# Kernel optimization log

Hardware: AMD Instinct MI355X
Metric: run time of the kernel (lower is better)

The kernel has to match this reference:

```python
import jax, jax.numpy as jnp
import numpy as np
import math

B, C, N, T = 16, 32, 500, 10
NH, DK = 8, 8
D = NH * DK  # 64
TT = 6       # tem_size after conv_temp1 (10->6)
EPS = 1e-5


def setup_inputs() -> dict:
    key = jax.random.key(0)
    ks = jax.random.split(key, 32)
    s = 0.05
    rn = lambda k, shp: jax.random.normal(k, shp, dtype=jnp.float32) * s
    return {
        "x": jax.random.normal(ks[0], (B, C, N, T), dtype=jnp.float32),
        "A": jax.random.uniform(ks[1], (N, N), dtype=jnp.float32) / N,
        "conv1_W": rn(ks[2], (32, 32)), "conv1_b": jnp.zeros((32,), jnp.float32),
        "te1_W": rn(ks[3], (64, 32)), "te1_b": jnp.zeros((64,), jnp.float32),
        "convq_W": rn(ks[4], (64, 64, 1, 3)), "convq_b": jnp.zeros((64,), jnp.float32),
        "convk_W": rn(ks[5], (64, 64, 1, 3)), "convk_b": jnp.zeros((64,), jnp.float32),
        "linv_W": rn(ks[6], (64, 64)), "linv_b": jnp.zeros((64,), jnp.float32),
        "lino_W": rn(ks[7], (64, 64)), "lino_b": jnp.zeros((64,), jnp.float32),
        "te2_W": rn(ks[8], (32, 64)), "te2_b": jnp.zeros((32,), jnp.float32),
        "mlp_W": rn(ks[9], (64, 160)), "mlp_b": jnp.zeros((64,), jnp.float32),
        "ct1_W": rn(ks[10], (6, 10)), "ct1_b": jnp.zeros((6,), jnp.float32),
        "tat_c1_W": rn(ks[11], (32,)), "tat_c2_W": rn(ks[12], (500,)),
        "tat_w": rn(ks[13], (500, 32)), "tat_b": jnp.zeros((6, 6), jnp.float32),
        "tat_v": rn(ks[14], (6, 6)),
        "bn1_g": jnp.ones((6,), jnp.float32), "bn1_b": jnp.zeros((6,), jnp.float32),
        "bn2_g": jnp.ones((32,), jnp.float32), "bn2_b": jnp.zeros((32,), jnp.float32),
    }


def _forward(x, A, conv1_W, conv1_b, te1_W, te1_b, convq_W, convq_b, convk_W, convk_b,
             linv_W, linv_b, lino_W, lino_b, te2_W, te2_b, mlp_W, mlp_b, ct1_W, ct1_b,
             tat_c1_W, tat_c2_W, tat_w, tat_b, tat_v, bn1_g, bn1_b, bn2_g, bn2_b):
    b, c, n, t = x.shape
    c1x1 = lambda z, W, bb: jnp.einsum('bchw,oc->bohw', z, W) + bb[None, :, None, None]
    residual = c1x1(x, conv1_W, conv1_b)                      # (B,32,N,T)
    h = c1x1(x, te1_W, te1_b)                                 # (B,64,N,T)
    # --- temporal-context multi-head self-attention (att bias is 0 in source due to bug) ---
    dn = ('NCHW', 'OIHW', 'NCHW')
    q = jax.lax.conv_general_dilated(h, convq_W, (1, 1), ((0, 0), (1, 1)), dimension_numbers=dn) + convq_b[None, :, None, None]
    k = jax.lax.conv_general_dilated(h, convk_W, (1, 1), ((0, 0), (1, 1)), dimension_numbers=dn) + convk_b[None, :, None, None]
    sh = lambda z: z.reshape(b, NH, DK, n, t).transpose(0, 3, 1, 4, 2)  # (B,N,h,T,dk)
    q, k = sh(q), sh(k)
    hp = h.transpose(0, 2, 3, 1)                              # (B,N,T,64)
    v = (hp @ linv_W.T + linv_b).reshape(b, n, t, NH, DK).transpose(0, 1, 3, 2, 4)
    p = jax.nn.softmax(jnp.einsum('bnhtd,bnhsd->bnhts', q, k) / math.sqrt(DK), axis=-1)
    o = jnp.einsum('bnhts,bnhsd->bnhtd', p, v).transpose(0, 1, 3, 2, 4).reshape(b, n, t, D)
    h = (o @ lino_W.T + lino_b).transpose(0, 3, 1, 2)         # (B,64,N,T)
    h = c1x1(h, te2_W, te2_b)                                 # (B,32,N,T)
    # --- multi_gcn_d: static adjacency diffusion + per-timestep attention adjacency ---
    co = h.shape[1]
    xt = h.transpose(0, 3, 2, 1)                              # (B,T,N,C)
    att = jax.nn.softmax(jnp.einsum('btnc,btmc->btnm', xt, xt) / math.sqrt(co), axis=-1)
    outs = [h]
    z = jnp.einsum('btvc,wv->btwc', xt, A); outs.append(z.transpose(0, 3, 2, 1))
    z = jnp.einsum('btvc,wv->btwc', z, A);  outs.append(z.transpose(0, 3, 2, 1))
    z = jnp.einsum('btvc,btwv->btwc', xt, att); outs.append(z.transpose(0, 3, 2, 1))
    z = jnp.einsum('btvc,btwv->btwc', z, att);  outs.append(z.transpose(0, 3, 2, 1))
    hc = c1x1(jnp.concatenate(outs, axis=1), mlp_W, mlp_b)    # (B,64,N,T)
    g = jnp.tanh(hc[:, :co]) * jax.nn.sigmoid(hc[:, co:])     # (B,32,N,10)
    # --- conv_temp1: 1x1 conv over the time axis, 10 -> 6 ---
    g = jnp.einsum('bcnt,st->bcns', g, ct1_W) + ct1_b[None, None, None, :]  # (B,32,N,6)
    # --- TATT_1 temporal attention coefficients ---
    f1 = jnp.einsum('bcnt,c->btn', g, tat_c1_W)               # (B,6,N)
    f2 = jnp.einsum('bcnt,n->bct', g, tat_c2_W)               # (B,32,6)
    logits = jax.nn.sigmoid(jnp.einsum('btn,nc,bcs->bts', f1, tat_w, f2) + tat_b)
    logits = jnp.einsum('pt,bts->bps', tat_v, logits)         # (B,6,6)
    lp = logits.transpose(0, 2, 1)
    mu = lp.mean((0, 2), keepdims=True); var = lp.var((0, 2), keepdims=True)
    lp = (lp - mu) / jnp.sqrt(var + EPS) * bn1_g[None, :, None] + bn1_b[None, :, None]
    coefs = jax.nn.softmax(lp.transpose(0, 2, 1), axis=-1)    # (B,6,6)
    Tc = coefs.transpose(0, 2, 1)
    xo = jnp.einsum('bcnl,blq->bcnq', g, Tc)                  # (B,32,N,6)
    xo = jnp.where(xo > 0, xo, 0.01 * xo) + residual[..., -xo.shape[-1]:]
    mu = xo.mean((0, 2, 3), keepdims=True); var = xo.var((0, 2, 3), keepdims=True)
    return (xo - mu) / jnp.sqrt(var + EPS) * bn2_g[None, :, None, None] + bn2_b[None, :, None, None]


def reference(x, A, conv1_W, conv1_b, te1_W, te1_b, convq_W, convq_b, convk_W, convk_b,
              linv_W, linv_b, lino_W, lino_b, te2_W, te2_b, mlp_W, mlp_b, ct1_W, ct1_b,
              tat_c1_W, tat_c2_W, tat_w, tat_b, tat_v, bn1_g, bn1_b, bn2_g, bn2_b):
    return _forward(x, A, conv1_W, conv1_b, te1_W, te1_b, convq_W, convq_b, convk_W, convk_b,
                    linv_W, linv_b, lino_W, lino_b, te2_W, te2_b, mlp_W, mlp_b, ct1_W, ct1_b,
                    tat_c1_W, tat_c2_W, tat_w, tat_b, tat_v, bn1_g, bn1_b, bn2_g, bn2_b)
```

## Files before the change

### kernel.cpp

```cpp
#include <hip/hip_runtime.h>

typedef unsigned short u16;
typedef unsigned int u32;

__device__ __forceinline__ float b2f(u16 v) { return __uint_as_float((u32)v << 16); }
__device__ __forceinline__ float lopart(u32 u) { return __uint_as_float(u << 16); }
__device__ __forceinline__ float hipart(u32 u) { return __uint_as_float(u & 0xffff0000u); }
__device__ __forceinline__ u16 f2b(float f) {
  u32 u = __float_as_uint(f);
  u32 r = u + 0x7fffu + ((u >> 16) & 1u);
  return (u16)(r >> 16);
}
__device__ __forceinline__ u32 pk2(float a, float b) {
  return (u32)f2b(a) | ((u32)f2b(b) << 16);
}
__device__ __forceinline__ u32 cvtpk(float lo, float hi) {
  u32 r;
  asm("v_cvt_pk_bf16_f32 %0, %1, %2" : "=v"(r) : "v"(lo), "v"(hi));
  return r;
}
__device__ __forceinline__ float rd(const void* p, int i, bool BF) {
  return BF ? b2f(((const u16*)p)[i]) : ((const float*)p)[i];
}

struct Ptrs { const void* p[29]; };

typedef __attribute__((ext_vector_type(8))) short short8;
typedef __attribute__((ext_vector_type(4))) float floatx4;

__global__ __launch_bounds__(256) void k_prep(Ptrs ps, float* __restrict__ Wf,
                                              u16* __restrict__ Abf, float* __restrict__ WT,
                                              u16* __restrict__ WBu, float* __restrict__ stats) {
  bool BF = ((*(const u32*)ps.p[25]) & 0xffffu) != 0;
  int blk = blockIdx.x, tid = threadIdx.x;
  if (blk < 256) {
    int j = blk * 256 + tid;
    if (j >= 65322) return;
    const int SZ[27] = {1024,32,2048,64,12288,64,12288,64,4096,64,4096,64,2048,32,
                        10240,64,60,6,32,500,16000,36,36,6,6,32,32};
    int t = 0, off = 0;
#pragma unroll
    for (int k = 0; k < 27; ++k) {
      if (t == k && j >= off + SZ[k]) { off += SZ[k]; t = k + 1; }
    }
    Wf[j] = rd(ps.p[2 + t], j - off, BF);
  } else if (blk < 1280) {
    int i = (blk - 256) * 256 + tid;
    int r = i >> 9, v = i & 511;
    bool in = (r < 500) && (v < 500);
    u16 o = 0;
    if (in) o = BF ? ((const u16*)ps.p[1])[r * 500 + v] : f2b(((const float*)ps.p[1])[r * 500 + v]);
    Abf[i] = o;
  } else if (blk < 1366) {
    int i = (blk - 1280) * 256 + tid;
    const void* p2  = ps.p[2];
    const void* p4  = ps.p[4];
    const void* p5  = ps.p[5];
    const void* p6  = ps.p[6];
    const void* p7  = ps.p[7];
    const void* p8  = ps.p[8];
    const void* p9  = ps.p[9];
    const void* p10 = ps.p[10];
    const void* p11 = ps.p[11];
    const void* p12 = ps.p[12];
    const void* p13 = ps.p[13];
    const void* p14 = ps.p[14];
    const void* p15 = ps.p[15];
    const void* p16 = ps.p[16];
    if (i < 1024) {
      WT[i] = rd(p2, (i & 31) * 32 + (i >> 5), BF);
    } else if (i < 7168) {
      int j2 = i - 1024;
      int o = j2 & 63, ct = j2 >> 6;
      int c = ct / 3, tap = ct - c * 3;
      float sq = 0.f, sk = 0.f;
      for (int i2 = 0; i2 < 64; ++i2) {
        float te = rd(p4, i2 * 32 + c, BF);
        sq += rd(p6, o * 192 + i2 * 3 + tap, BF) * te;
        sk += rd(p8, o * 192 + i2 * 3 + tap, BF) * te;
      }
      ((u32*)WT)[i] = pk2(sq, sk);
    } else if (i < 7552) {
      int j2 = i - 7168;
      int f = j2 >> 6, o = j2 & 63;
      const void* pw = (f & 1) ? p8 : p6;
      float S0 = 0.f, S1 = 0.f, S2 = 0.f;
      for (int i2 = 0; i2 < 64; ++i2) {
        float tb = rd(p5, i2, BF);
        S0 += rd(pw, o * 192 + i2 * 3 + 0, BF) * tb;
        S1 += rd(pw, o * 192 + i2 * 3 + 1, BF) * tb;
        S2 += rd(pw, o * 192 + i2 * 3 + 2, BF) * tb;
      }
      float r;
      if (f == 0)      r = rd(p7, o, BF) + S0 + S1 + S2;
      else if (f == 1) r = rd(p9, o, BF) + S0 + S1 + S2;
      else if (f < 4)  r = S0;
      else             r = S2;
      WT[i] = r;
    } else if (i < 9600) {
      int j2 = i - 7552;
      int c = j2 >> 6, o = j2 & 63;
      float s = 0.f;
      for (int i2 = 0; i2 < 64; ++i2)
        s += rd(p10, o * 64 + i2, BF) * rd(p4, i2 * 32 + c, BF);
      WT[i] = s;
    } else if (i < 9664) {
      int o = i - 9600;
      float s = rd(p11, o, BF);
      for (int i2 = 0; i2 < 64; ++i2)
        s += rd(p10, o * 64 + i2, BF) * rd(p5, i2, BF);
      WT[i] = s;
    } else if (i < 11712) {
      int j2 = i - 9664;
      int jj = j2 >> 5, c = j2 & 31;
      float s = 0.f;
      for (int o2 = 0; o2 < 64; ++o2)
        s += rd(p14, c * 64 + o2, BF) * rd(p12, o2 * 64 + jj, BF);
      WT[i] = s;
    } else if (i < 11744) {
      int c = i - 11712;
      float s = rd(p15, c, BF);
      for (int o2 = 0; o2 < 64; ++o2)
        s += rd(p14, c * 64 + o2, BF) * rd(p13, o2, BF);
      WT[i] = s;
    } else if (i < 21984) {
      int j2 = i - 11744;
      int j = j2 & 7, lanev = (j2 >> 3) & 63, ct = (j2 >> 9) & 3, kt = j2 >> 11;
      int qv = lanev >> 4, lnv = lanev & 15;
      int o = ct * 16 + lnv, k = kt * 32 + qv * 8 + j;
      WBu[j2] = f2b(rd(p16, o * 160 + k, BF));
    }
  } else {
    if (tid < 64) stats[tid] = 0.f;
  }
}

__global__ __launch_bounds__(256, 4) void k_a2m(const u16* __restrict__ Abf,
                                                u16* __restrict__ A2bf) {
  __shared__ u32 blsT[8192];
  int tid = threadIdx.x;
  int c0 = blockIdx.x * 32;
  for (int i = tid; i < 8192; i += 256) {
    int c = i & 31, h = i >> 5;
    int r0 = 2 * h;
    u32 lo = Abf[r0 * 512 + c0 + c];
    u32 hi = Abf[(r0 + 1) * 512 + c0 + c];
    blsT[c * 256 + (((h & 0xFC) ^ ((c & 15) << 2)) | (h & 3))] = lo | (hi << 16);
  }
  __syncthreads();
  int lane = tid & 63, wave = tid >> 6;
  int q = lane >> 4, ln = lane & 15;
  int rbase = blockIdx.y * 64 + wave * 16;
  const u32* Au = (const u32*)Abf;
  int arow = (rbase + ln) * 256;
  union F8 { u32 u[4]; short8 s; };
  floatx4 acc[2] = {{0.f,0.f,0.f,0.f},{0.f,0.f,0.f,0.f}};
  for (int c2 = 0; c2 < 16; ++c2) {
    int hb = c2 * 16 + q * 4;
    F8 af;
#pragma unroll
    for (int i2 = 0; i2 < 4; ++i2) af.u[i2] = Au[arow + hb + i2];
#pragma unroll
    for (int t2 = 0; t2 < 2; ++t2) {
      int c = t2 * 16 + ln;
      int baseT = c * 256 + (hb ^ ((c & 15) << 2));
      F8 bf;
#pragma unroll
      for (int i2 = 0; i2 < 4; ++i2) bf.u[i2] = blsT[baseT + i2];
      acc[t2] = __builtin_amdgcn_mfma_f32_16x16x32_bf16(af.s, bf.s, acc[t2], 0, 0, 0);
    }
  }
#pragma unroll
  for (int t2 = 0; t2 < 2; ++t2) {
#pragma unroll
    for (int i2 = 0; i2 < 4; ++i2) {
      int r = rbase + q * 4 + i2;
      A2bf[r * 512 + c0 + t2 * 16 + ln] = f2b(acc[t2][i2]);
    }
  }
}

__global__ __launch_bounds__(256, 7) void k_front3(
    const void* __restrict__ xraw, const void* __restrict__ g1, const float* __restrict__ WT,
    const float* __restrict__ c1B,
    float* __restrict__ h3x, float* __restrict__ res6)
{
  __shared__ __align__(16) float arena[4][1440];
  int tid = threadIdx.x;
  int wave = tid >> 6, lane = tid & 63;
  float* Aw = arena[wave];
  int pair = blockIdx.x * 4 + wave;
  int b = pair / 500, n = pair - b * 500;

  const float* c1T  = WT;
  const u32*   qkF  = (const u32*)(WT + 1024);
  const float* bCq  = WT + 7168;
  const float* bCk  = WT + 7232;
  const float* bE0q = WT + 7296;
  const float* bE0k = WT + 7360;
  const float* bE2q = WT + 7424;
  const float* bE2k = WT + 7488;
  const float* vT   = WT + 7552;
  const float* bvp  = WT + 9600;
  const float* otT  = WT + 9664;
  const float* botp = WT + 11712;

  {
    bool BF = ((*(const u32*)g1) & 0xffffu) != 0;
    int c0 = lane >> 1, hf = (lane & 1) * 5;
    int base = ((b * 32 + c0) * 500 + n) * 10 + hf;
    float* dst = Aw + c0 * 12 + hf;
    if (BF) {
      const u16* xp = (const u16*)xraw + base;
#pragma unroll
      for (int k2 = 0; k2 < 5; ++k2) dst[k2] = b2f(xp[k2]);
    } else {
      const float* xp = (const float*)xraw + base;
#pragma unroll
      for (int k2 = 0; k2 < 5; ++k2) dst[k2] = xp[k2];
    }
  }
  __builtin_amdgcn_wave_barrier();

  int cl = lane & 31, th = lane >> 5;

  {
    float r0 = c1B[cl], r1 = r0, r2 = r0;
#pragma unroll 4
    for (int i = 0; i < 32; ++i) {
      float w = c1T[i * 32 + cl];
      const float* xr = Aw + i * 12 + 4 + th * 3;
      r0 += w * xr[0]; r1 += w * xr[1]; r2 += w * xr[2];
    }
    float* rp = res6 + ((b * 32 + cl) * 500 + n) * 6 + th * 3;
    rp[0] = r0; rp[1] = r1; rp[2] = r2;
  }

  float qr[10], kr[10], vr[10];
  {
    float cq = bCq[lane], ck = bCk[lane], bv = bvp[lane];
#pragma unroll
    for (int t = 0; t < 10; ++t) { qr[t] = cq; kr[t] = ck; vr[t] = bv; }
    qr[0] -= bE0q[lane]; kr[0] -= bE0k[lane];
    qr[9] -= bE2q[lane]; kr[9] -= bE2k[lane];
    const u32* qp0 = qkF + lane;
    const float* vp0 = vT + lane;
#pragma unroll 2
    for (int c = 0; c < 32; ++c) {
      const float* xr = Aw + c * 12;
      float4 ha = *(const float4*)xr;
      float4 hb = *(const float4*)(xr + 4);
      float2 hc = *(const float2*)(xr + 8);
      u32 u0 = qp0[c * 192];
      u32 u1 = qp0[c * 192 + 64];
      u32 u2 = qp0[c * 192 + 128];
      float wv = vp0[c * 64];
      float q0 = lopart(u0), q1 = lopart(u1), q2 = lopart(u2);
      float k0 = hipart(u0), k1 = hipart(u1), k2v = hipart(u2);
      float hh[10] = {ha.x, ha.y, ha.z, ha.w, hb.x, hb.y, hb.z, hb.w, hc.x, hc.y};
#pragma unroll
      for (int t = 0; t < 10; ++t) { float c_ = hh[t]; qr[t] += q1 * c_; kr[t] += k1 * c_; vr[t] += wv * c_; }
#pragma unroll
      for (int t = 1; t < 10; ++t) { float c_ = hh[t - 1]; qr[t] += q0 * c_; kr[t] += k0 * c_; }
#pragma unroll
      for (int t = 0; t < 9; ++t) { float c_ = hh[t + 1]; qr[t] += q2 * c_; kr[t] += k2v * c_; }
    }
  }
  __builtin_amdgcn_wave_barrier();
  {
    u32* qu = (u32*)Aw + lane * 5;
    u32* ku = (u32*)Aw + 320 + lane * 5;
#pragma unroll
    for (int m = 0; m < 5; ++m) {
      qu[m] = cvtpk(qr[2 * m], qr[2 * m + 1]);
      ku[m] = cvtpk(kr[2 * m], kr[2 * m + 1]);
    }
  }
  __builtin_amdgcn_wave_barrier();

  {
    const u32* qb = (const u32*)Aw;
    const u32* kb = (const u32*)Aw + 320;
#pragma unroll
    for (int pass = 0; pass < 2; ++pass) {
      int row = pass * 64 + lane;
      if (row < 80) {
        int h8 = (row / 10) * 8, r = row - (row / 10) * 10;
        int rm = r >> 1, rs = r & 1;
        float sv[10];
#pragma unroll
        for (int s = 0; s < 10; ++s) sv[s] = 0.f;
#pragma unroll 2
        for (int d = 0; d < 8; ++d) {
          int jj = h8 + d;
          u32 qu = qb[jj * 5 + rm];
          float qv = rs ? hipart(qu) : lopart(qu);
          const u32* kp2 = kb + jj * 5;
          u32 ka0 = kp2[0], ka1 = kp2[1], ka2 = kp2[2], ka3 = kp2[3], ka4 = kp2[4];
          sv[0] += qv * lopart(ka0); sv[1] += qv * hipart(ka0);
          sv[2] += qv * lopart(ka1); sv[3] += qv * hipart(ka1);
          sv[4] += qv * lopart(ka2); sv[5] += qv * hipart(ka2);
          sv[6] += qv * lopart(ka3); sv[7] += qv * hipart(ka3);
          sv[8] += qv * lopart(ka4); sv[9] += qv * hipart(ka4);
        }
        const float sc_ = 0.35355339059327373f;
        float mx = sv[0];
#pragma unroll
        for (int s = 1; s < 10; ++s) mx = fmaxf(mx, sv[s]);
        float tot = 0.f, ev[10];
#pragma unroll
        for (int s = 0; s < 10; ++s) { ev[s] = __expf((sv[s] - mx) * sc_); tot += ev[s]; }
        float inv = 1.f / tot;
        float* pp = Aw + 640 + row * 10;
#pragma unroll
        for (int s = 0; s < 10; ++s) pp[s] = ev[s] * inv;
      }
    }
  }
  __builtin_amdgcn_wave_barrier();

  {
    const float* pb = Aw + 640 + (lane >> 3) * 100;
    float orr[10];
#pragma unroll
    for (int t = 0; t < 10; ++t) {
      const float* pr = pb + t * 10;
      float a = 0.f;
#pragma unroll
      for (int s = 0; s < 10; ++s) a += pr[s] * vr[s];
      orr[t] = a;
    }
    float* op = Aw + lane * 12;
    *(float4*)op       = make_float4(orr[0], orr[1], orr[2], orr[3]);
    *(float4*)(op + 4) = make_float4(orr[4], orr[5], orr[6], orr[7]);
    *(float2*)(op + 8) = make_float2(orr[8], orr[9]);
  }
  __builtin_amdgcn_wave_barrier();

  {
    float bt2 = botp[cl];
    float a5[5];
#pragma unroll
    for (int k2 = 0; k2 < 5; ++k2) a5[k2] = bt2;
    const float* tp0 = otT + cl;
    const float* base = Aw + th * 5;
#pragma unroll 2
    for (int j = 0; j < 64; ++j) {
      float w = tp0[j * 32];
      const float* lp = base + j * 12;
#pragma unroll
      for (int k2 = 0; k2 < 5; ++k2) a5[k2] += w * lp[k2];
    }
    int t0 = th * 5;
#pragma unroll
    for (int k2 = 0; k2 < 5; ++k2)
      h3x[((b * 10 + t0 + k2) * 500 + n) * 32 + cl] = a5[k2];
  }
}

__global__ __launch_bounds__(256, 4) void k_z12m(const float* __restrict__ h3x,
    const u16* __restrict__ Abf, const u16* __restrict__ A2bf,
    float* __restrict__ z1x, float* __restrict__ z2x) {
  __shared__ u32 xlsT[8192];
  int tid = threadIdx.x, bt = blockIdx.x;
  const float* src = h3x + bt * 16000;
  for (int i = tid; i < 8192; i += 256) {
    int n = i & 31, h = i >> 5;
    int r0 = 2 * h;
    float v0 = (r0 < 500) ? src[r0 * 32 + n] : 0.f;
    float v1 = (r0 + 1 < 500) ? src[(r0 + 1) * 32 + n] : 0.f;
    xlsT[n * 256 + (((h & 0xFC) ^ ((n & 15) << 2)) | (h & 3))] = cvtpk(v0, v1);
  }
  __syncthreads();
  int lane = tid & 63, wave = tid >> 6;
  int q = lane >> 4, ln = lane & 15;
  int rbase = blockIdx.y * 64 + wave * 16;
  const u32* Au = (const u32*)Abf;
  const u32* A2u = (const u32*)A2bf;
  int arow = (rbase + ln) * 256;
  union F8 { u32 u[4]; short8 s; };
  floatx4 acc1[2] = {{0.f,0.f,0.f,0.f},{0.f,0.f,0.f,0.f}};
  floatx4 acc2[2] = {{0.f,0.f,0.f,0.f},{0.f,0.f,0.f,0.f}};
  for (int c2 = 0; c2 < 16; ++c2) {
    int hb = c2 * 16 + q * 4;
    F8 a1f, a2f;
#pragma unroll
    for (int i2 = 0; i2 < 4; ++i2) {
      a1f.u[i2] = Au[arow + hb + i2];
      a2f.u[i2] = A2u[arow + hb + i2];
    }
#pragma unroll
    for (int t2 = 0; t2 < 2; ++t2) {
      int n = t2 * 16 + ln;
      int baseT = n * 256 + (hb ^ ((n & 15) << 2));
      F8 bf;
#pragma unroll
      for (int i2 = 0; i2 < 4; ++i2) bf.u[i2] = xlsT[baseT + i2];
      acc1[t2] = __builtin_amdgcn_mfma_f32_16x16x32_bf16(a1f.s, bf.s, acc1[t2], 0, 0, 0);
      acc2[t2] = __builtin_amdgcn_mfma_f32_16x16x32_bf16(a2f.s, bf.s, acc2[t2], 0, 0, 0);
    }
  }
  int outb = bt * 16000;
#pragma unroll
  for (int t2 = 0; t2 < 2; ++t2) {
#pragma unroll
    for (int i2 = 0; i2 < 4; ++i2) {
      int r = rbase + q * 4 + i2;
      if (r < 500) {
        z1x[outb + r * 32 + t2 * 16 + ln] = acc1[t2][i2];
        z2x[outb + r * 32 + t2 * 16 + ln] = acc2[t2][i2];
      }
    }
  }
}

__global__ __launch_bounds__(256, 2) void k_attn2(const float* __restrict__ keys,
                                                  const float* __restrict__ vals,
                                                  float* __restrict__ outp) {
  __shared__ u32 kls[10240];
  __shared__ u32 vls[8192];
  __shared__ u32 aux[1216];
  int tid = threadIdx.x, bt = blockIdx.x, yh = blockIdx.y;
  const float* kb = keys + bt * 16000;
  const float* vb = vals + bt * 16000;
  for (int i = tid; i < 8192; i += 256) {
    int r = i >> 4, cu = i & 15;
    float2 g = make_float2(0.f, 0.f);
    if (r < 500) g = *(const float2*)(kb + r * 32 + cu * 2);
    kls[r * 20 + cu] = cvtpk(g.x, g.y);
    int n = i & 31, h = i >> 5;
    int r0 = 2 * h;
    float v0 = (r0 < 500) ? vb[r0 * 32 + n] : 0.f;
    float v1 = (r0 + 1 < 500) ? vb[(r0 + 1) * 32 + n] : 0.f;
    vls[n * 256 + (((h & 0xFC) ^ ((n & 15) << 2)) | (h & 3))] = cvtpk(v0, v1);
  }
  __syncthreads();
  int lane = tid & 63, wave = tid >> 6;
  int q = lane >> 4, ln = lane & 15;
  int wrow = wave >> 1, ch = wave & 1;
  float* smx = (float*)(aux + 1088);
  float* sms = (float*)(aux + 1152);
  u32* myp = aux + wave * 272;
  float* zex = (float*)aux;
  u16* pw = (u16*)myp;
  union F8 { u32 u[4]; short8 s; };
  const float sc = 0.17677669529663687f;
  int outb = bt * 16000;
  for (int chunk = 0; chunk < 8; ++chunk) {
    int rbase = yh * 256 + chunk * 32 + wrow * 16;
    F8 af;
    {
      int r = rbase + ln;
      int wbase = r * 20 + q * 4;
#pragma unroll
      for (int i2 = 0; i2 < 4; ++i2)
        af.u[i2] = kls[wbase + i2];
    }
    floatx4 acc[16];
#pragma unroll
    for (int ctl = 0; ctl < 16; ++ctl) {
      int r2 = (ch * 16 + ctl) * 16 + ln;
      int wb2 = r2 * 20 + q * 4;
      F8 bf;
#pragma unroll
      for (int i2 = 0; i2 < 4; ++i2)
        bf.u[i2] = kls[wb2 + i2];
      acc[ctl] = __builtin_amdgcn_mfma_f32_16x16x32_bf16(af.s, bf.s,
                (floatx4){0.f, 0.f, 0.f, 0.f}, 0, 0, 0);
    }
    if (ch == 1 && ln >= 4) {
#pragma unroll
      for (int i2 = 0; i2 < 4; ++i2) acc[15][i2] = -1e30f;
    }
    float m[4];
#pragma unroll
    for (int i2 = 0; i2 < 4; ++i2) {
      float mm = -1e30f;
#pragma unroll
      for (int ctl = 0; ctl < 16; ++ctl) mm = fmaxf(mm, acc[ctl][i2]);
#pragma unroll
      for (int d = 1; d < 16; d <<= 1) mm = fmaxf(mm, __shfl_xor(mm, d));
      m[i2] = mm;
    }
    if (ln == 0) {
#pragma unroll
      for (int i2 = 0; i2 < 4; ++i2) smx[wave * 16 + q * 4 + i2] = m[i2];
    }
    __syncthreads();
    float sp[4];
#pragma unroll
    for (int i2 = 0; i2 < 4; ++i2) {
      float mm = fmaxf(m[i2], smx[(wave ^ 1) * 16 + q * 4 + i2]);
      float s = 0.f;
#pragma unroll
      for (int ctl = 0; ctl < 16; ++ctl) {
        float e = __expf((acc[ctl][i2] - mm) * sc);
        acc[ctl][i2] = e; s += e;
      }
#pragma unroll
      for (int d = 1; d < 16; d <<= 1) s += __shfl_xor(s, d);
      sp[i2] = s;
    }
    if (ln == 0) {
#pragma unroll
      for (int i2 = 0; i2 < 4; ++i2) sms[wave * 16 + q * 4 + i2] = sp[i2];
    }
    __syncthreads();
    float inv[4];
#pragma unroll
    for (int i2 = 0; i2 < 4; ++i2)
      inv[i2] = 1.f / (sp[i2] + sms[(wave ^ 1) * 16 + q * 4 + i2]);
    floatx4 zacc[2] = {{0.f,0.f,0.f,0.f},{0.f,0.f,0.f,0.f}};
    for (int c2l = 0; c2l < 8; ++c2l) {
#pragma unroll
      for (int t2 = 0; t2 < 2; ++t2) {
        int ctl = c2l * 2 + t2;
#pragma unroll
        for (int i2 = 0; i2 < 4; ++i2)
          pw[(q * 4 + i2) * 34 + t2 * 16 + ln] = f2b(acc[ctl][i2]);
      }
      __builtin_amdgcn_wave_barrier();
      F8 pa;
#pragma unroll
      for (int i2 = 0; i2 < 4; ++i2) pa.u[i2] = myp[ln * 17 + q * 4 + i2];
      int hb = (ch * 8 + c2l) * 16 + q * 4;
#pragma unroll
      for (int t2 = 0; t2 < 2; ++t2) {
        int n = t2 * 16 + ln;
        int baseT = n * 256 + (hb ^ ((n & 15) << 2));
        F8 bf;
#pragma unroll
        for (int i2 = 0; i2 < 4; ++i2) bf.u[i2] = vls[baseT + i2];
        zacc[t2] = __builtin_amdgcn_mfma_f32_16x16x32_bf16(pa.s, bf.s, zacc[t2], 0, 0, 0);
      }
      __builtin_amdgcn_wave_barrier();
    }
    __syncthreads();
    if (ch) {
#pragma unroll
      for (int t2 = 0; t2 < 2; ++t2)
#pragma unroll
        for (int i2 = 0; i2 < 4; ++i2)
          zex[wrow * 544 + (q * 4 + i2) * 34 + t2 * 16 + ln] = zacc[t2][i2];
    }
    __syncthreads();
    if (!ch) {
#pragma unroll
      for (int t2 = 0; t2 < 2; ++t2) {
#pragma unroll
        for (int i2 = 0; i2 < 4; ++i2) {
          int r = rbase + q * 4 + i2;
          if (r < 500) {
            float vsum = zacc[t2][i2] + zex[wrow * 544 + (q * 4 + i2) * 34 + t2 * 16 + ln];
            outp[outb + r * 32 + t2 * 16 + ln] = vsum * inv[i2];
          }
        }
      }
    }
  }
}

__global__ __launch_bounds__(256, 2) void k_gate(
    const float* __restrict__ h3x, const float* __restrict__ z1x, const float* __restrict__ z2x,
    const float* __restrict__ z3x, const float* __restrict__ z4x,
    const u32* __restrict__ WBq, const float* __restrict__ mlpB,
    const float* __restrict__ ct1W, const float* __restrict__ ct1B,
    float* __restrict__ g2w)
{
  __shared__ u32 wlds[5120];
  int tid = threadIdx.x;
  for (int i = tid; i < 5120; i += 256) wlds[i] = WBq[i];
  __syncthreads();
  int lane = tid & 63, wave = tid >> 6;
  int q = lane >> 4, ln = lane & 15;
  int b = blockIdx.y;
  int n0 = blockIdx.x * 32 + wave * 8;
  int nA = n0 + (ln & 7);
  int tAb = ln >> 3;
  int nD = n0 + (q & 1) * 4;
  int tDb = q >> 1;
  float g2a[4][2][6];
#pragma unroll
  for (int i = 0; i < 4; ++i)
#pragma unroll
    for (int ch = 0; ch < 2; ++ch)
#pragma unroll
      for (int s = 0; s < 6; ++s) g2a[i][ch][s] = 0.f;
  float bias[4];
#pragma unroll
  for (int ct = 0; ct < 4; ++ct) bias[ct] = mlpB[ct * 16 + ln];
  union F8 { u32 u[4]; short8 s; };
  for (int tile = 0; tile < 5; ++tile) {
    int tA = tile * 2 + tAb;
    int offA = (((b * 10 + tA) * 500) + nA) * 32 + q * 8;
    floatx4 acc[4];
#pragma unroll
    for (int ct = 0; ct < 4; ++ct) acc[ct] = (floatx4){bias[ct], bias[ct], bias[ct], bias[ct]};
#pragma unroll
    for (int kt = 0; kt < 5; ++kt) {
      const float* sp = kt == 0 ? h3x : kt == 1 ? z1x : kt == 2 ? z2x : kt == 3 ? z3x : z4x;
      float4 a0 = *(const float4*)(sp + offA);
      float4 a1 = *(const float4*)(sp + offA + 4);
      F8 af;
      af.u[0] = cvtpk(a0.x, a0.y);
      af.u[1] = cvtpk(a0.z, a0.w);
      af.u[2] = cvtpk(a1.x, a1.y);
      af.u[3] = cvtpk(a1.z, a1.w);
#pragma unroll
      for (int ct = 0; ct < 4; ++ct) {
        F8 bfr;
        const u32* wp = wlds + (((kt * 4 + ct) << 6) + lane) * 4;
#pragma unroll
        for (int i2 = 0; i2 < 4; ++i2) bfr.u[i2] = wp[i2];
        acc[ct] = __builtin_amdgcn_mfma_f32_16x16x32_bf16(af.s, bfr.s, acc[ct], 0, 0, 0);
      }
    }
    int tD = tile * 2 + tDb;
    float c6[6];
#pragma unroll
    for (int s = 0; s < 6; ++s) c6[s] = ct1W[s * 10 + tD];
#pragma unroll
    for (int i = 0; i < 4; ++i) {
      float e0 = __expf(2.f * acc[0][i]);
      float g0 = ((e0 - 1.f) / (e0 + 1.f)) * (1.f / (1.f + __expf(-acc[2][i])));
      float e1 = __expf(2.f * acc[1][i]);
      float g1 = ((e1 - 1.f) / (e1 + 1.f)) * (1.f / (1.f + __expf(-acc[3][i])));
#pragma unroll
      for (int s = 0; s < 6; ++s) {
        g2a[i][0][s] += g0 * c6[s];
        g2a[i][1][s] += g1 * c6[s];
      }
    }
  }
#pragma unroll
  for (int i = 0; i < 4; ++i)
#pragma unroll
    for (int ch = 0; ch < 2; ++ch)
#pragma unroll
      for (int s = 0; s < 6; ++s)
        g2a[i][ch][s] += __shfl_xor(g2a[i][ch][s], 32);
  if (q < 2) {
#pragma unroll
    for (int i = 0; i < 4; ++i) {
      int n = nD + i;
      if (n < 500) {
#pragma unroll
        for (int ch = 0; ch < 2; ++ch) {
          int c = ln + ch * 16;
          float* gp = g2w + ((b * 32 + c) * 500 + n) * 6;
#pragma unroll
          for (int s = 0; s < 6; ++s) gp[s] = g2a[i][ch][s] + ct1B[s];
        }
      }
    }
  }
}

__global__ __launch_bounds__(256) void k_f12(const float* __restrict__ g2w,
                                             const float* __restrict__ tc1W,
                                             const float* __restrict__ c2W,
                                             float* __restrict__ f1w, float* __restrict__ f2w) {
  int blk = blockIdx.x, tid = threadIdx.x;
  if (blk < 188) {
    int i = blk * 256 + tid;
    if (i >= 48000) return;
    int b = i / 3000, rem = i - b * 3000, s = rem / 500, n = rem - s * 500;
    float a = 0.f;
    for (int c = 0; c < 32; ++c) a += g2w[((b * 32 + c) * 500 + n) * 6 + s] * tc1W[c];
    f1w[(b * 6 + s) * 500 + n] = a;
  } else {
    int pb = (blk - 188) * 4 + (tid >> 6);
    int b = pb >> 5, c = pb & 31, lane = tid & 63;
    float acc[6];
#pragma unroll
    for (int t = 0; t < 6; ++t) acc[t] = 0.f;
    for (int n = lane; n < 500; n += 64) {
      float w = c2W[n];
      const float* gp = g2w + ((b * 32 + c) * 500 + n) * 6;
#pragma unroll
      for (int t = 0; t < 6; ++t) acc[t] += w * gp[t];
    }
#pragma unroll
    for (int t = 0; t < 6; ++t)
      for (int off = 32; off; off >>= 1) acc[t] += __shfl_xor(acc[t], off);
    if (lane == 0) {
#pragma unroll
      for (int t = 0; t < 6; ++t) f2w[(b * 32 + c) * 6 + t] = acc[t];
    }
  }
}

__global__ __launch_bounds__(256) void k_tatt(
    const float* __restrict__ f1w, const float* __restrict__ tatw,
    const float* __restrict__ f2w, const float* __restrict__ tatb, const float* __restrict__ tatv,
    float* __restrict__ lg2w)
{
  __shared__ float mid[192];
  __shared__ float lgt[36];
  int b = blockIdx.x, tid = threadIdx.x;
  if (tid < 192) {
    int t = tid >> 5, c = tid & 31;
    float a = 0.f;
    const float* f1p = f1w + (b * 6 + t) * 500;
    for (int n = 0; n < 500; ++n) a += f1p[n] * tatw[n * 32 + c];
    mid[t * 32 + c] = a;
  }
  __syncthreads();
  if (tid < 36) {
    int t = tid / 6, s = tid - t * 6;
    float a = tatb[t * 6 + s];
    for (int c = 0; c < 32; ++c) a += mid[t * 32 + c] * f2w[(b * 32 + c) * 6 + s];
    lgt[t * 6 + s] = 1.f / (1.f + expf(-a));
  }
  __syncthreads();
  if (tid < 36) {
    int p = tid / 6, s = tid - p * 6;
    float a = 0.f;
#pragma unroll
    for (int t2 = 0; t2 < 6; ++t2) a += tatv[p * 6 + t2] * lgt[t2 * 6 + s];
    lg2w[(b * 6 + p) * 6 + s] = a;
  }
}

__global__ __launch_bounds__(128) void k_coefs(const float* __restrict__ lg2w,
    const float* __restrict__ bn1g, const float* __restrict__ bn1b, float* __restrict__ tcw) {
  __shared__ float mu[6], iv[6], gg[6], bb[6];
  int tid = threadIdx.x;
  if (tid < 6) {
    float s = 0.f, sq = 0.f;
    for (int b = 0; b < 16; ++b)
      for (int q = 0; q < 6; ++q) {
        float v = lg2w[(b * 6 + q) * 6 + tid];
        s += v; sq += v * v;
      }
    float m = s / 96.f;
    mu[tid] = m;
    iv[tid] = rsqrtf(sq / 96.f - m * m + 1e-5f);
    gg[tid] = bn1g[tid]; bb[tid] = bn1b[tid];
  }
  __syncthreads();
  for (int idx = tid; idx < 96; idx += 128) {
    int b = idx / 6, q = idx - b * 6;
    float v[6], mx = -1e30f;
#pragma unroll
    for (int l = 0; l < 6; ++l) {
      v[l] = (lg2w[(b * 6 + q) * 6 + l] - mu[l]) * iv[l] * gg[l] + bb[l];
      mx = fmaxf(mx, v[l]);
    }
    float tot = 0.f;
#pragma unroll
    for (int l = 0; l < 6; ++l) { v[l] = expf(v[l] - mx); tot += v[l]; }
    float inv = 1.f / tot;
#pragma unroll
    for (int l = 0; l < 6; ++l) tcw[(b * 6 + l) * 6 + q] = v[l] * inv;
  }
}

__global__ __launch_bounds__(256) void k_xo(const float* __restrict__ g2w,
    const float* __restrict__ res6, const float* __restrict__ tcw,
    float* __restrict__ xow, float* __restrict__ stats) {
  __shared__ float Tcl[36];
  __shared__ float redS[32][8], redQ[32][8];
  int b = blockIdx.x, chunk = blockIdx.y, tid = threadIdx.x;
  if (tid < 36) Tcl[tid] = tcw[b * 36 + tid];
  __syncthreads();
  int c = tid & 31, sub = tid >> 5;
  int n0 = chunk * 50;
  float s = 0.f, sq = 0.f;
  for (int idx = sub; idx < 300; idx += 8) {
    int nl = idx / 6, q = idx - nl * 6;
    int n = n0 + nl;
    int base = ((b * 32 + c) * 500 + n) * 6;
    const float* gp = g2w + base;
    float xv = 0.f;
#pragma unroll
    for (int l = 0; l < 6; ++l) xv += gp[l] * Tcl[l * 6 + q];
    xv = xv > 0.f ? xv : 0.01f * xv;
    xv += res6[base + q];
    xow[base + q] = xv;
    s += xv; sq += xv * xv;
  }
  redS[c][sub] = s; redQ[c][sub] = sq;
  __syncthreads();
  if (sub == 0) {
    float ts = 0.f, tq = 0.f;
#pragma unroll
    for (int k = 0; k < 8; ++k) { ts += redS[c][k]; tq += redQ[c][k]; }
    atomicAdd(&stats[c], ts);
    atomicAdd(&stats[32 + c], tq);
  }
}

__global__ __launch_bounds__(256) void k_out(const float* __restrict__ xow,
    const float* __restrict__ stats, const float* __restrict__ g2c, const float* __restrict__ b2c,
    float* __restrict__ out) {
  int base = (blockIdx.x * 256 + threadIdx.x) * 4;
#pragma unroll
  for (int k = 0; k < 4; ++k) {
    int i = base + k;
    int c = (i / 3000) & 31;
    float m = stats[c] * (1.f / 48000.f);
    float var = stats[32 + c] * (1.f / 48000.f) - m * m;
    out[i] = (xow[i] - m) * rsqrtf(var + 1e-5f) * g2c[c] + b2c[c];
  }
}

extern "C" void kernel_launch(void* const* d_in, const int* in_sizes, int n_in,
                              void* d_out, int out_size, void* d_ws, size_t ws_size,
                              hipStream_t stream)
{
  (void)in_sizes; (void)out_size;

  float* ws = (float*)d_ws;
  float* Af   = ws;
  float* Wf   = Af + 250000;
  float* A2   = Wf + 65536;
  float* h3x  = A2 + 250000;
  float* z1x  = h3x + 2560000;
  float* z2x  = z1x + 2560000;
  float* z3x  = z2x + 2560000;
  float* z4x  = z3x + 2560000;
  float* res6 = z4x + 2560000;
  float* g2w  = res6 + 1536000;
  float* f1w  = g2w + 1536000;
  float* f2w  = f1w + 48000;
  float* lg2w = f2w + 3072;
  float* tcw  = lg2w + 576;
  float* stats= tcw + 576;
  float* xow  = z1x;
  u16*   Abf  = (u16*)g2w;
  u16*   A2bf = (u16*)(g2w + 131072);
  float* WTp  = g2w + 262144;
  u16*   WBu  = (u16*)f1w;
  if (ws_size < (size_t)16489952 * sizeof(float)) return;

  const float* c1B  = Wf + 1024;
  const float* mlpB = Wf + 48512;
  const float* ct1W = Wf + 48576;
  const float* ct1B = Wf + 48636;
  const float* tc1W = Wf + 48642;
  const float* tc2W = Wf + 48674;
  const float* tatw = Wf + 49174;
  const float* tatb = Wf + 65174;
  const float* tatv = Wf + 65210;
  const float* bn1g = Wf + 65246;
  const float* bn1b = Wf + 65252;
  const float* bn2g = Wf + 65258;
  const float* bn2b = Wf + 65290;

  Ptrs ps;
  for (int i = 0; i < 29; ++i) ps.p[i] = (i < n_in) ? d_in[i] : d_in[0];

  k_prep <<<dim3(1367),    256, 0, stream>>>(ps, Wf, Abf, WTp, WBu, stats);
  k_a2m  <<<dim3(16, 8),   256, 0, stream>>>(Abf, A2bf);
  k_front3<<<dim3(2000),   256, 0, stream>>>(ps.p[0], ps.p[25], WTp, c1B, h3x, res6);
  k_z12m <<<dim3(160, 8),  256, 0, stream>>>(h3x, Abf, A2bf, z1x, z2x);
  k_attn2<<<dim3(160, 2),  256, 0, stream>>>(h3x, h3x, z3x);
  k_attn2<<<dim3(160, 2),  256, 0, stream>>>(h3x, z3x, z4x);
  k_gate <<<dim3(16, 16),  256, 0, stream>>>(h3x, z1x, z2x, z3x, z4x,
                                             (const u32*)WBu, mlpB, ct1W, ct1B, g2w);
  k_f12  <<<dim3(316),     256, 0, stream>>>(g2w, tc1W, tc2W, f1w, f2w);
  k_tatt <<<dim3(16),      256, 0, stream>>>(f1w, tatw, f2w, tatb, tatv, lg2w);
  k_coefs<<<dim3(1),       128, 0, stream>>>(lg2w, bn1g, bn1b, tcw);
  k_xo   <<<dim3(16, 10),  256, 0, stream>>>(g2w, res6, tcw, xow, stats);
  k_out  <<<dim3(1500),    256, 0, stream>>>(xow, stats, bn2g, bn2b, (float*)d_out);
}
```

Measured before the change: 401.1 us.

## Compute front Q/K/V projections with bf16 MFMA instead of scalar FMA loops

Replaces the per-lane scalar FMA accumulation of the fused te1+conv_q/conv_k/linear_v projections in k_front3 with 16x16x32 bf16 MFMA tiles. It does this by building a time-shifted im2col of x in LDS, while k_prep emits the projection weights pre-swizzled into MFMA fragment layout along with per-boundary bias classes. Attention probabilities and V are now stored as bf16 in LDS. Shared memory grows and the occupancy hint drops from 7 to 5 blocks. The change adds bf16 rounding of Q/K/V inputs and probabilities.

```diff
diff --git a/kernel.cpp b/kernel.cpp
--- a/kernel.cpp
+++ b/kernel.cpp
@@ -33,6 +33,20 @@
                                               u16* __restrict__ WBu, float* __restrict__ stats) {
   bool BF = ((*(const u32*)ps.p[25]) & 0xffffu) != 0;
   int blk = blockIdx.x, tid = threadIdx.x;
+  const void* p2  = ps.p[2];
+  const void* p4  = ps.p[4];
+  const void* p5  = ps.p[5];
+  const void* p6  = ps.p[6];
+  const void* p7  = ps.p[7];
+  const void* p8  = ps.p[8];
+  const void* p9  = ps.p[9];
+  const void* p10 = ps.p[10];
+  const void* p11 = ps.p[11];
+  const void* p12 = ps.p[12];
+  const void* p13 = ps.p[13];
+  const void* p14 = ps.p[14];
+  const void* p15 = ps.p[15];
+  const void* p16 = ps.p[16];
   if (blk < 256) {
     int j = blk * 256 + tid;
     if (j >= 65322) return;
@@ -53,82 +67,77 @@
     Abf[i] = o;
   } else if (blk < 1366) {
     int i = (blk - 1280) * 256 + tid;
-    const void* p2  = ps.p[2];
-    const void* p4  = ps.p[4];
-    const void* p5  = ps.p[5];
-    const void* p6  = ps.p[6];
-    const void* p7  = ps.p[7];
-    const void* p8  = ps.p[8];
-    const void* p9  = ps.p[9];
-    const void* p10 = ps.p[10];
-    const void* p11 = ps.p[11];
-    const void* p12 = ps.p[12];
-    const void* p13 = ps.p[13];
-    const void* p14 = ps.p[14];
-    const void* p15 = ps.p[15];
-    const void* p16 = ps.p[16];
     if (i < 1024) {
       WT[i] = rd(p2, (i & 31) * 32 + (i >> 5), BF);
-    } else if (i < 7168) {
-      int j2 = i - 1024;
-      int o = j2 & 63, ct = j2 >> 6;
-      int c = ct / 3, tap = ct - c * 3;
-      float sq = 0.f, sk = 0.f;
-      for (int i2 = 0; i2 < 64; ++i2) {
-        float te = rd(p4, i2 * 32 + c, BF);
-        sq += rd(p6, o * 192 + i2 * 3 + tap, BF) * te;
-        sk += rd(p8, o * 192 + i2 * 3 + tap, BF) * te;
-      }
-      ((u32*)WT)[i] = pk2(sq, sk);
-    } else if (i < 7552) {
-      int j2 = i - 7168;
-      int f = j2 >> 6, o = j2 & 63;
-      const void* pw = (f & 1) ? p8 : p6;
-      float S0 = 0.f, S1 = 0.f, S2 = 0.f;
-      for (int i2 = 0; i2 < 64; ++i2) {
-        float tb = rd(p5, i2, BF);
-        S0 += rd(pw, o * 192 + i2 * 3 + 0, BF) * tb;
-        S1 += rd(pw, o * 192 + i2 * 3 + 1, BF) * tb;
-        S2 += rd(pw, o * 192 + i2 * 3 + 2, BF) * tb;
-      }
-      float r;
-      if (f == 0)      r = rd(p7, o, BF) + S0 + S1 + S2;
-      else if (f == 1) r = rd(p9, o, BF) + S0 + S1 + S2;
-      else if (f < 4)  r = S0;
-      else             r = S2;
-      WT[i] = r;
-    } else if (i < 9600) {
-      int j2 = i - 7552;
-      int c = j2 >> 6, o = j2 & 63;
-      float s = 0.f;
-      for (int i2 = 0; i2 < 64; ++i2)
-        s += rd(p10, o * 64 + i2, BF) * rd(p4, i2 * 32 + c, BF);
-      WT[i] = s;
-    } else if (i < 9664) {
+    } else if (i >= 9600 && i < 9664) {
       int o = i - 9600;
       float s = rd(p11, o, BF);
       for (int i2 = 0; i2 < 64; ++i2)
         s += rd(p10, o * 64 + i2, BF) * rd(p5, i2, BF);
       WT[i] = s;
-    } else if (i < 11712) {
+    } else if (i >= 9664 && i < 11712) {
       int j2 = i - 9664;
       int jj = j2 >> 5, c = j2 & 31;
       float s = 0.f;
       for (int o2 = 0; o2 < 64; ++o2)
         s += rd(p14, c * 64 + o2, BF) * rd(p12, o2 * 64 + jj, BF);
       WT[i] = s;
-    } else if (i < 11744) {
+    } else if (i >= 11712 && i < 11744) {
       int c = i - 11712;
       float s = rd(p15, c, BF);
       for (int o2 = 0; o2 < 64; ++o2)
         s += rd(p14, c * 64 + o2, BF) * rd(p13, o2, BF);
       WT[i] = s;
-    } else if (i < 21984) {
+    } else if (i >= 11744 && i < 21984) {
       int j2 = i - 11744;
       int j = j2 & 7, lanev = (j2 >> 3) & 63, ct = (j2 >> 9) & 3, kt = j2 >> 11;
       int qv = lanev >> 4, lnv = lanev & 15;
       int o = ct * 16 + lnv, k = kt * 32 + qv * 8 + j;
       WBu[j2] = f2b(rd(p16, o * 160 + k, BF));
+    }
+  } else if (blk < 1390) {
+    int idx = (blk - 1366) * 256 + tid;
+    int i2 = idx & 3, lanev = (idx >> 2) & 63, mt = (idx >> 8) & 7, ks = idx >> 11;
+    int q2 = lanev >> 4, ln = lanev & 15;
+    int o = (mt & 3) * 16 + ln;
+    const void* src = (mt >= 4) ? p8 : p6;
+    int kb0 = q2 * 8 + 2 * i2;
+    float v0 = 0.f, v1 = 0.f;
+    for (int i3 = 0; i3 < 64; ++i3) {
+      float w = rd(src, o * 192 + i3 * 3 + ks, BF);
+      v0 += w * rd(p4, i3 * 32 + kb0, BF);
+      v1 += w * rd(p4, i3 * 32 + kb0 + 1, BF);
+    }
+    ((u32*)WT)[22016 + idx] = pk2(v0, v1);
+  } else if (blk < 1394) {
+    int idx = (blk - 1390) * 256 + tid;
+    int i2 = idx & 3, lanev = (idx >> 2) & 63, mt = idx >> 8;
+    int o = mt * 16 + (lanev & 15);
+    int kb0 = (lanev >> 4) * 8 + 2 * i2;
+    float v0 = 0.f, v1 = 0.f;
+    for (int i3 = 0; i3 < 64; ++i3) {
+      float w = rd(p10, o * 64 + i3, BF);
+      v0 += w * rd(p4, i3 * 32 + kb0, BF);
+      v1 += w * rd(p4, i3 * 32 + kb0 + 1, BF);
+    }
+    ((u32*)WT)[28160 + idx] = pk2(v0, v1);
+  } else if (blk < 1397) {
+    int j = (blk - 1394) * 256 + tid;
+    if (j < 768) {
+      bool isK = j >= 384;
+      int jj = isK ? j - 384 : j;
+      int cls = jj >> 6, o = jj & 63;
+      const void* srcW = isK ? p8 : p6;
+      const void* srcB = isK ? p9 : p7;
+      float S0 = 0.f, S1 = 0.f, S2 = 0.f;
+      for (int i3 = 0; i3 < 64; ++i3) {
+        float tb = rd(p5, i3, BF);
+        S0 += rd(srcW, o * 192 + i3 * 3 + 0, BF) * tb;
+        S1 += rd(srcW, o * 192 + i3 * 3 + 1, BF) * tb;
+        S2 += rd(srcW, o * 192 + i3 * 3 + 2, BF) * tb;
+      }
+      float val = rd(srcB, o, BF) + S1 + (cls > 0 ? S0 : 0.f) + (cls < 2 ? S2 : 0.f);
+      WT[29184 + j] = val;
     }
   } else {
     if (tid < 64) stats[tid] = 0.f;
@@ -180,12 +189,12 @@
   }
 }
 
-__global__ __launch_bounds__(256, 7) void k_front3(
+__global__ __launch_bounds__(256, 5) void k_front3(
     const void* __restrict__ xraw, const void* __restrict__ g1, const float* __restrict__ WT,
     const float* __restrict__ c1B,
     float* __restrict__ h3x, float* __restrict__ res6)
 {
-  __shared__ __align__(16) float arena[4][1440];
+  __shared__ __align__(16) float arena[4][1680];
   int tid = threadIdx.x;
   int wave = tid >> 6, lane = tid & 63;
   float* Aw = arena[wave];
@@ -193,17 +202,13 @@
   int b = pair / 500, n = pair - b * 500;
 
   const float* c1T  = WT;
-  const u32*   qkF  = (const u32*)(WT + 1024);
-  const float* bCq  = WT + 7168;
-  const float* bCk  = WT + 7232;
-  const float* bE0q = WT + 7296;
-  const float* bE0k = WT + 7360;
-  const float* bE2q = WT + 7424;
-  const float* bE2k = WT + 7488;
-  const float* vT   = WT + 7552;
   const float* bvp  = WT + 9600;
   const float* otT  = WT + 9664;
   const float* botp = WT + 11712;
+  const u32* WQKf = (const u32*)WT + 22016;
+  const u32* WVf  = (const u32*)WT + 28160;
+  const float* bq3 = WT + 29184;
+  const float* bk3 = WT + 29568;
 
   {
     bool BF = ((*(const u32*)g1) & 0xffffu) != 0;
@@ -223,6 +228,7 @@
   __builtin_amdgcn_wave_barrier();
 
   int cl = lane & 31, th = lane >> 5;
+  int q2 = lane >> 4, ln15 = lane & 15;
 
   {
     float r0 = c1B[cl], r1 = r0, r2 = r0;
@@ -236,44 +242,79 @@
     rp[0] = r0; rp[1] = r1; rp[2] = r2;
   }
 
-  float qr[10], kr[10], vr[10];
   {
-    float cq = bCq[lane], ck = bCk[lane], bv = bvp[lane];
-#pragma unroll
-    for (int t = 0; t < 10; ++t) { qr[t] = cq; kr[t] = ck; vr[t] = bv; }
-    qr[0] -= bE0q[lane]; kr[0] -= bE0k[lane];
-    qr[9] -= bE2q[lane]; kr[9] -= bE2k[lane];
-    const u32* qp0 = qkF + lane;
-    const float* vp0 = vT + lane;
-#pragma unroll 2
-    for (int c = 0; c < 32; ++c) {
-      const float* xr = Aw + c * 12;
-      float4 ha = *(const float4*)xr;
-      float4 hb = *(const float4*)(xr + 4);
-      float2 hc = *(const float2*)(xr + 8);
-      u32 u0 = qp0[c * 192];
-      u32 u1 = qp0[c * 192 + 64];
-      u32 u2 = qp0[c * 192 + 128];
-      float wv = vp0[c * 64];
-      float q0 = lopart(u0), q1 = lopart(u1), q2 = lopart(u2);
-      float k0 = hipart(u0), k1 = hipart(u1), k2v = hipart(u2);
-      float hh[10] = {ha.x, ha.y, ha.z, ha.w, hb.x, hb.y, hb.z, hb.w, hc.x, hc.y};
-#pragma unroll
-      for (int t = 0; t < 10; ++t) { float c_ = hh[t]; qr[t] += q1 * c_; kr[t] += k1 * c_; vr[t] += wv * c_; }
-#pragma unroll
-      for (int t = 1; t < 10; ++t) { float c_ = hh[t - 1]; qr[t] += q0 * c_; kr[t] += k0 * c_; }
-#pragma unroll
-      for (int t = 0; t < 9; ++t) { float c_ = hh[t + 1]; qr[t] += q2 * c_; kr[t] += k2v * c_; }
+    u32* xT3u = (u32*)Aw + 384;
+    for (int e = lane; e < 480; e += 64) {
+      int t = e / 48, col2 = e - t * 48;
+      int kk0 = col2 * 2, kk1 = kk0 + 1;
+      int tau0 = kk0 >> 5, c0 = kk0 & 31;
+      int tau1 = kk1 >> 5, c1 = kk1 & 31;
+      int tx0 = t - 1 + tau0, tx1 = t - 1 + tau1;
+      float f0 = (tx0 >= 0 && tx0 < 10) ? Aw[c0 * 12 + tx0] : 0.f;
+      float f1 = (tx1 >= 0 && tx1 < 10) ? Aw[c1 * 12 + tx1] : 0.f;
+      xT3u[t * 52 + col2] = cvtpk(f0, f1);
     }
   }
   __builtin_amdgcn_wave_barrier();
+
+  union F8 { u32 u[4]; short8 s; };
+  floatx4 aq[4] = {{0.f,0.f,0.f,0.f},{0.f,0.f,0.f,0.f},{0.f,0.f,0.f,0.f},{0.f,0.f,0.f,0.f}};
+  floatx4 ak[4] = {{0.f,0.f,0.f,0.f},{0.f,0.f,0.f,0.f},{0.f,0.f,0.f,0.f},{0.f,0.f,0.f,0.f}};
+  floatx4 av[4] = {{0.f,0.f,0.f,0.f},{0.f,0.f,0.f,0.f},{0.f,0.f,0.f,0.f},{0.f,0.f,0.f,0.f}};
   {
-    u32* qu = (u32*)Aw + lane * 5;
-    u32* ku = (u32*)Aw + 320 + lane * 5;
-#pragma unroll
-    for (int m = 0; m < 5; ++m) {
-      qu[m] = cvtpk(qr[2 * m], qr[2 * m + 1]);
-      ku[m] = cvtpk(kr[2 * m], kr[2 * m + 1]);
+    const u32* xT3u = (const u32*)Aw + 384;
+#pragma unroll
+    for (int ks = 0; ks < 3; ++ks) {
+      F8 bfr;
+      const u32* bp = xT3u + ln15 * 52 + ks * 16 + q2 * 4;
+#pragma unroll
+      for (int i2 = 0; i2 < 4; ++i2) bfr.u[i2] = bp[i2];
+#pragma unroll
+      for (int mt = 0; mt < 4; ++mt) {
+        F8 afr;
+        const u32* ap = WQKf + ((ks * 8 + mt) * 64 + lane) * 4;
+#pragma unroll
+        for (int i2 = 0; i2 < 4; ++i2) afr.u[i2] = ap[i2];
+        aq[mt] = __builtin_amdgcn_mfma_f32_16x16x32_bf16(afr.s, bfr.s, aq[mt], 0, 0, 0);
+      }
+#pragma unroll
+      for (int mt = 0; mt < 4; ++mt) {
+        F8 afr;
+        const u32* ap = WQKf + ((ks * 8 + 4 + mt) * 64 + lane) * 4;
+#pragma unroll
+        for (int i2 = 0; i2 < 4; ++i2) afr.u[i2] = ap[i2];
+        ak[mt] = __builtin_amdgcn_mfma_f32_16x16x32_bf16(afr.s, bfr.s, ak[mt], 0, 0, 0);
+      }
+      if (ks == 1) {
+#pragma unroll
+        for (int mt = 0; mt < 4; ++mt) {
+          F8 afr;
+          const u32* ap = WVf + (mt * 64 + lane) * 4;
+#pragma unroll
+          for (int i2 = 0; i2 < 4; ++i2) afr.u[i2] = ap[i2];
+          av[mt] = __builtin_amdgcn_mfma_f32_16x16x32_bf16(afr.s, bfr.s, av[mt], 0, 0, 0);
+        }
+      }
+    }
+  }
+  __builtin_amdgcn_wave_barrier();
+  if (ln15 < 10) {
+    int t = ln15;
+    int cls = (t == 0) ? 0 : ((t == 9) ? 2 : 1);
+    const float* bq = bq3 + cls * 64;
+    const float* bk = bk3 + cls * 64;
+    u16* q16 = (u16*)Aw;
+    u16* k16 = (u16*)((u32*)Aw + 320);
+    u16* v16 = (u16*)((u32*)Aw + 960);
+#pragma unroll
+    for (int mt = 0; mt < 4; ++mt) {
+#pragma unroll
+      for (int i2 = 0; i2 < 4; ++i2) {
+        int o = mt * 16 + q2 * 4 + i2;
+        q16[o * 10 + t] = f2b(aq[mt][i2] + bq[o]);
+        k16[o * 10 + t] = f2b(ak[mt][i2] + bk[o]);
+        v16[o * 10 + t] = f2b(av[mt][i2] + bvp[o]);
+      }
     }
   }
   __builtin_amdgcn_wave_barrier();
@@ -311,23 +352,34 @@
 #pragma unroll
         for (int s = 0; s < 10; ++s) { ev[s] = __expf((sv[s] - mx) * sc_); tot += ev[s]; }
         float inv = 1.f / tot;
-        float* pp = Aw + 640 + row * 10;
-#pragma unroll
-        for (int s = 0; s < 10; ++s) pp[s] = ev[s] * inv;
+        u32* pp = (u32*)Aw + 1280 + row * 5;
+#pragma unroll
+        for (int m2 = 0; m2 < 5; ++m2)
+          pp[m2] = cvtpk(ev[2 * m2] * inv, ev[2 * m2 + 1] * inv);
       }
     }
   }
   __builtin_amdgcn_wave_barrier();
 
   {
-    const float* pb = Aw + 640 + (lane >> 3) * 100;
+    float vrL[10];
+    const u32* vp = (const u32*)Aw + 960 + lane * 5;
+#pragma unroll
+    for (int m2 = 0; m2 < 5; ++m2) {
+      u32 w = vp[m2];
+      vrL[2 * m2] = lopart(w); vrL[2 * m2 + 1] = hipart(w);
+    }
+    const u32* pb = (const u32*)Aw + 1280 + (lane >> 3) * 50;
     float orr[10];
 #pragma unroll
     for (int t = 0; t < 10; ++t) {
-      const float* pr = pb + t * 10;
+      const u32* pr = pb + t * 5;
       float a = 0.f;
 #pragma unroll
-      for (int s = 0; s < 10; ++s) a += pr[s] * vr[s];
+      for (int m2 = 0; m2 < 5; ++m2) {
+        u32 w = pr[m2];
+        a += lopart(w) * vrL[2 * m2] + hipart(w) * vrL[2 * m2 + 1];
+      }
       orr[t] = a;
     }
     float* op = Aw + lane * 12;
@@ -851,7 +903,7 @@
   Ptrs ps;
   for (int i = 0; i < 29; ++i) ps.p[i] = (i < n_in) ? d_in[i] : d_in[0];
 
-  k_prep <<<dim3(1367),    256, 0, stream>>>(ps, Wf, Abf, WTp, WBu, stats);
+  k_prep <<<dim3(1398),    256, 0, stream>>>(ps, Wf, Abf, WTp, WBu, stats);
   k_a2m  <<<dim3(16, 8),   256, 0, stream>>>(Abf, A2bf);
   k_front3<<<dim3(2000),   256, 0, stream>>>(ps.p[0], ps.p[25], WTp, c1B, h3x, res6);
   k_z12m <<<dim3(160, 8),  256, 0, stream>>>(h3x, Abf, A2bf, z1x, z2x);
```

New measurement: 391.9 us. -2.3%, faster.
